# Performance work log

Hardware: AMD Instinct MI355X
Metric: run time of the kernel (lower is better)

## Reference

```python
import jax, jax.numpy as jnp
import numpy as np

B, I, H = 256, 512, 512

def setup_inputs() -> dict:
    key = jax.random.key(0)
    ks = jax.random.split(key, 12)
    u = lambda k, s: jax.random.uniform(k, s, dtype=jnp.float32)
    inp = {
        'inputs': jax.random.normal(ks[0], (B, I), dtype=jnp.float32),
        'state': jax.random.normal(ks[1], (B, H), dtype=jnp.float32),
        'sensory_mu': u(ks[2], (I, H)) * 0.5 + 0.3,
        'sensory_sigma': u(ks[3], (I, H)) * 5.0 + 3.0,
        'sensory_W': u(ks[4], (I, H)) * 0.99 + 0.01,
        'sensory_erev': (2.0 * jax.random.randint(ks[5], (I, H), 0, 2) - 1.0).astype(jnp.float32),
        'mu': u(ks[6], (H, H)) * 0.5 + 0.3,
        'sigma': u(ks[7], (H, H)) * 5.0 + 3.0,
        'W': u(ks[8], (H, H)) * 0.99 + 0.01,
        'erev': (2.0 * jax.random.randint(ks[9], (H, H), 0, 2) - 1.0).astype(jnp.float32),
        'vleak': u(ks[10], (H,)) * 0.4 - 0.2,
        'gleak': jnp.ones((H,), dtype=jnp.float32),
        'cm': jnp.full((H,), 0.5, dtype=jnp.float32),
    }
    return inp


def reference(inputs, state, sensory_mu, sensory_sigma, sensory_W, sensory_erev,
              mu, sigma, W, erev, vleak, gleak, cm):
    eps = 1e-08
    # sensory synapses: (B, I, H) broadcast
    s_act = jax.nn.sigmoid((inputs[:, :, None] - sensory_mu[None]) * sensory_sigma[None])
    s_w_act = sensory_W * s_act                      # (B, I, H)
    w_num_s = jnp.sum(s_w_act * sensory_erev, axis=1)  # (B, H)
    w_den_s = jnp.sum(s_w_act, axis=1)                 # (B, H)
    # inter-neuron synapses: (B, H, H) broadcast
    i_act = jax.nn.sigmoid((state[:, :, None] - mu[None]) * sigma[None])
    i_w_act = W * i_act                               # (B, H, H)
    w_num_i = jnp.sum(i_w_act * erev, axis=1)         # (B, H)
    w_den_i = jnp.sum(i_w_act, axis=1)                # (B, H)
    w_numerator = w_num_i + w_num_s
    w_denominator = w_den_i + w_den_s
    G_total = gleak + w_denominator
    tau = cm / (G_total + eps)
    numerator = cm * state + gleak * vleak + w_numerator
    denominator = cm + G_total
    v_inf = numerator / (denominator + eps)
    dt = 0.1
    next_state = v_inf + (state - v_inf) * jnp.exp(-dt / (tau + eps))
    return jnp.tanh(next_state)
```

## Files before the change

kernel.cpp:

```cpp
#include <hip/hip_runtime.h>
#include <stdint.h>

constexpr int NB = 256;
constexpr int NI = 512;
constexpr int NH = 512;

constexpr int TB    = 8;
constexpr int NT    = 32;
constexpr int CHUNK = 32;
constexpr int NSPL  = 32;
constexpr int HBLK  = 256;

__device__ __constant__ const float SC0 =  0.24781886f;
__device__ __constant__ const float SC1 = -0.01739900f;
__device__ __constant__ const float SC2 =  9.68558e-4f;
__device__ __constant__ const float SC3 = -3.09967e-5f;
__device__ __constant__ const float SC4 =  5.03772e-7f;
__device__ __constant__ const float SC5 = -3.21180e-9f;

__global__ __launch_bounds__(256, 6) void ltc_accum(
    const float* __restrict__ inputs,
    const float* __restrict__ state,
    const float* __restrict__ smu, const float* __restrict__ ssg,
    const float* __restrict__ sW,  const float* __restrict__ ser,
    const float* __restrict__ imu, const float* __restrict__ isg,
    const float* __restrict__ iW,  const float* __restrict__ ier,
    float* __restrict__ wsNum, float* __restrict__ wsDen)
{
    __shared__ float xs[CHUNK][TB];

    const int bi    = blockIdx.x;
    const int sigma = bi & (NSPL - 1);
    const int btile = (bi >> 5) & (NT - 1);
    const int hhalf = bi >> 10;
    const int b0 = btile * TB;
    const int h  = hhalf * HBLK + threadIdx.x;

    const bool sens = sigma < 16;
    const int  r0   = (sens ? sigma : sigma - 16) * CHUNK;

    const float* __restrict__ src  = sens ? inputs : state;
    const float* __restrict__ Pmu  = sens ? smu : imu;
    const float* __restrict__ Psg  = sens ? ssg : isg;
    const float* __restrict__ PW   = sens ? sW  : iW;
    const float* __restrict__ Per  = sens ? ser : ier;

    {
        const int ii = threadIdx.x >> 3, bb = threadIdx.x & (TB - 1);
        xs[ii][bb] = src[(b0 + bb) * 512 + r0 + ii];
    }
    __syncthreads();

    float numA[TB], denA[TB];
#pragma unroll
    for (int bb = 0; bb < TB; ++bb) { numA[bb] = 0.f; denA[bb] = 0.f; }
    float sWsum = 0.f, sWesum = 0.f;

#pragma unroll 2
    for (int ii = 0; ii < CHUNK; ++ii) {
        const int p = (r0 + ii) * NH + h;
        const float a  = Psg[p];
        const float c  = Pmu[p] * a;
        const float W  = PW[p];
        const float We = W * Per[p];
        sWsum  += W;
        sWesum += We;
#pragma unroll
        for (int bb = 0; bb < TB; ++bb) {
            const float z  = __builtin_fmaf(xs[ii][bb], a, -c);
            const float zc = fminf(fmaxf(z, -7.0f), 7.0f);
            const float s  = zc * zc;
            float pl = __builtin_fmaf(SC5, s, SC4);
            pl = __builtin_fmaf(pl, s, SC3);
            pl = __builtin_fmaf(pl, s, SC2);
            pl = __builtin_fmaf(pl, s, SC1);
            pl = __builtin_fmaf(pl, s, SC0);
            const float g = zc * pl;
            denA[bb] = __builtin_fmaf(W,  g, denA[bb]);
            numA[bb] = __builtin_fmaf(We, g, numA[bb]);
        }
    }

#pragma unroll
    for (int bb = 0; bb < TB; ++bb) {
        const float den = __builtin_fmaf(0.5f, sWsum,  denA[bb]);
        const float num = __builtin_fmaf(0.5f, sWesum, numA[bb]);
        unsafeAtomicAdd(&wsNum[(b0 + bb) * NH + h], num);
        unsafeAtomicAdd(&wsDen[(b0 + bb) * NH + h], den);
    }
}

__global__ __launch_bounds__(256) void ltc_epilogue(
    const float* __restrict__ state,
    const float* __restrict__ vleak, const float* __restrict__ gleak,
    const float* __restrict__ cm,
    const float* __restrict__ wsNum, const float* __restrict__ wsDen,
    float* __restrict__ out)
{
    const int t = blockIdx.x * 256 + threadIdx.x;
    const int h = t & (NH - 1);
    const float st = state[t];
    const float gl = gleak[h];
    const float vl = vleak[h];
    const float c  = cm[h];
    const float wnum = wsNum[t];
    const float wden = wsDen[t];
    const float eps = 1e-8f;
    const float G = gl + wden;
    const float tau = c / (G + eps);
    const float numerator = c * st + gl * vl + wnum;
    const float denominator = c + G;
    const float v_inf = numerator / (denominator + eps);
    const float next = v_inf + (st - v_inf) * expf(-0.1f / (tau + eps));
    out[t] = tanhf(next);
}

extern "C" void kernel_launch(void* const* d_in, const int* in_sizes, int n_in,
                              void* d_out, int out_size, void* d_ws, size_t ws_size,
                              hipStream_t stream) {
    const float* inputs = (const float*)d_in[0];
    const float* state  = (const float*)d_in[1];
    const float* smu    = (const float*)d_in[2];
    const float* ssg    = (const float*)d_in[3];
    const float* sW     = (const float*)d_in[4];
    const float* ser    = (const float*)d_in[5];
    const float* imu    = (const float*)d_in[6];
    const float* isg    = (const float*)d_in[7];
    const float* iW     = (const float*)d_in[8];
    const float* ier    = (const float*)d_in[9];
    const float* vleak  = (const float*)d_in[10];
    const float* gleak  = (const float*)d_in[11];
    const float* cm     = (const float*)d_in[12];

    float* wsNum = (float*)d_ws;
    float* wsDen = wsNum + NB * NH;

    hipMemsetAsync(d_ws, 0, 2ull * NB * NH * sizeof(float), stream);

    ltc_accum<<<dim3(NSPL * NT * 2), dim3(256), 0, stream>>>(
        inputs, state, smu, ssg, sW, ser, imu, isg, iW, ier, wsNum, wsDen);
    ltc_epilogue<<<dim3(NB * NH / 256), dim3(256), 0, stream>>>(
        state, vleak, gleak, cm, wsNum, wsDen, (float*)d_out);
}
```

Measured before the change: 123.2 us.

## Pack synapse parameters into float4 with precomputed mu*sigma and W*erev

Adds a pre-pass kernel that interleaves sigma, mu*sigma, W and W*erev into one float4 array per side, so the accumulate kernel issues a single 16-byte load per row instead of four scalar loads plus two multiplies. It also replaces the min/max clamp with a med3 builtin. The pack runs on every call, adding an extra read of all parameters and a 8 MB write to workspace, plus one more launch.

```diff
diff --git a/kernel.cpp b/kernel.cpp
--- a/kernel.cpp
+++ b/kernel.cpp
@@ -10,6 +10,7 @@
 constexpr int CHUNK = 32;
 constexpr int NSPL  = 32;
 constexpr int HBLK  = 256;
+constexpr int SIDE_ELEMS = 512 * 512;
 
 __device__ __constant__ const float SC0 =  0.24781886f;
 __device__ __constant__ const float SC1 = -0.01739900f;
@@ -18,13 +19,41 @@
 __device__ __constant__ const float SC4 =  5.03772e-7f;
 __device__ __constant__ const float SC5 = -3.21180e-9f;
 
-__global__ __launch_bounds__(256, 6) void ltc_accum(
-    const float* __restrict__ inputs,
-    const float* __restrict__ state,
+__device__ __forceinline__ float clamp7(float z) {
+#if __has_builtin(__builtin_amdgcn_fmed3f)
+    return __builtin_amdgcn_fmed3f(z, -7.0f, 7.0f);
+#else
+    return fminf(fmaxf(z, -7.0f), 7.0f);
+#endif
+}
+
+__global__ __launch_bounds__(256) void ltc_pack(
     const float* __restrict__ smu, const float* __restrict__ ssg,
     const float* __restrict__ sW,  const float* __restrict__ ser,
     const float* __restrict__ imu, const float* __restrict__ isg,
     const float* __restrict__ iW,  const float* __restrict__ ier,
+    float4* __restrict__ ppk)
+{
+    const int side = blockIdx.x >> 10;
+    const int e    = (blockIdx.x & 1023) * 256 + threadIdx.x;
+    const float* mu = side ? imu : smu;
+    const float* sg = side ? isg : ssg;
+    const float* W  = side ? iW  : sW;
+    const float* er = side ? ier : ser;
+    const float a  = sg[e];
+    const float w  = W[e];
+    float4 p;
+    p.x = a;
+    p.y = mu[e] * a;
+    p.z = w;
+    p.w = w * er[e];
+    ppk[side * SIDE_ELEMS + e] = p;
+}
+
+__global__ __launch_bounds__(256, 6) void ltc_accum(
+    const float* __restrict__ inputs,
+    const float* __restrict__ state,
+    const float4* __restrict__ ppk,
     float* __restrict__ wsNum, float* __restrict__ wsDen)
 {
     __shared__ float xs[CHUNK][TB];
@@ -39,11 +68,8 @@
     const bool sens = sigma < 16;
     const int  r0   = (sens ? sigma : sigma - 16) * CHUNK;
 
-    const float* __restrict__ src  = sens ? inputs : state;
-    const float* __restrict__ Pmu  = sens ? smu : imu;
-    const float* __restrict__ Psg  = sens ? ssg : isg;
-    const float* __restrict__ PW   = sens ? sW  : iW;
-    const float* __restrict__ Per  = sens ? ser : ier;
+    const float*  __restrict__ src = sens ? inputs : state;
+    const float4* __restrict__ Pp  = ppk + (sens ? 0 : SIDE_ELEMS);
 
     {
         const int ii = threadIdx.x >> 3, bb = threadIdx.x & (TB - 1);
@@ -58,17 +84,14 @@
 
 #pragma unroll 2
     for (int ii = 0; ii < CHUNK; ++ii) {
-        const int p = (r0 + ii) * NH + h;
-        const float a  = Psg[p];
-        const float c  = Pmu[p] * a;
-        const float W  = PW[p];
-        const float We = W * Per[p];
+        const float4 P = Pp[(r0 + ii) * NH + h];
+        const float a = P.x, c = P.y, W = P.z, We = P.w;
         sWsum  += W;
         sWesum += We;
 #pragma unroll
         for (int bb = 0; bb < TB; ++bb) {
             const float z  = __builtin_fmaf(xs[ii][bb], a, -c);
-            const float zc = fminf(fmaxf(z, -7.0f), 7.0f);
+            const float zc = clamp7(z);
             const float s  = zc * zc;
             float pl = __builtin_fmaf(SC5, s, SC4);
             pl = __builtin_fmaf(pl, s, SC3);
@@ -132,13 +155,16 @@
     const float* gleak  = (const float*)d_in[11];
     const float* cm     = (const float*)d_in[12];
 
-    float* wsNum = (float*)d_ws;
-    float* wsDen = wsNum + NB * NH;
+    float4* ppk   = (float4*)d_ws;
+    float*  wsNum = (float*)((char*)d_ws + 2ull * SIDE_ELEMS * sizeof(float4));
+    float*  wsDen = wsNum + NB * NH;
 
-    hipMemsetAsync(d_ws, 0, 2ull * NB * NH * sizeof(float), stream);
+    hipMemsetAsync((void*)wsNum, 0, 2ull * NB * NH * sizeof(float), stream);
 
+    ltc_pack<<<dim3(2048), dim3(256), 0, stream>>>(
+        smu, ssg, sW, ser, imu, isg, iW, ier, ppk);
     ltc_accum<<<dim3(NSPL * NT * 2), dim3(256), 0, stream>>>(
-        inputs, state, smu, ssg, sW, ser, imu, isg, iW, ier, wsNum, wsDen);
+        inputs, state, ppk, wsNum, wsDen);
     ltc_epilogue<<<dim3(NB * NH / 256), dim3(256), 0, stream>>>(
         state, vleak, gleak, cm, wsNum, wsDen, (float*)d_out);
 }
```

New measurement: 129.4 us. +5.0%, slower.

## Replace atomic accumulation with per-split partial buffers reduced in epilogue

Applied to the files above, without the earlier changes.

Drops the workspace memset and the float atomics. Each split block now writes its (num, den) partial sums as a float2 into its own workspace slice, and the epilogue sums the S slices before the final state update. The split count is picked from the workspace size, and blocks loop over several chunks when S is below 32. It also uses fmed3 for the clamp and raises the launch-bounds occupancy hint to 8. The cost is extra partial-buffer traffic, which can reach 32 MB of writes and reads when S is 32.

```diff
diff --git a/kernel.cpp b/kernel.cpp
--- a/kernel.cpp
+++ b/kernel.cpp
@@ -2,13 +2,11 @@
 #include <stdint.h>
 
 constexpr int NB = 256;
-constexpr int NI = 512;
 constexpr int NH = 512;
+constexpr int NTGT = NB * NH;
 
 constexpr int TB    = 8;
-constexpr int NT    = 32;
 constexpr int CHUNK = 32;
-constexpr int NSPL  = 32;
 constexpr int HBLK  = 256;
 
 __device__ __constant__ const float SC0 =  0.24781886f;
@@ -18,93 +16,115 @@
 __device__ __constant__ const float SC4 =  5.03772e-7f;
 __device__ __constant__ const float SC5 = -3.21180e-9f;
 
-__global__ __launch_bounds__(256, 6) void ltc_accum(
+__device__ __forceinline__ float clamp7(float z) {
+#if __has_builtin(__builtin_amdgcn_fmed3f)
+    return __builtin_amdgcn_fmed3f(z, -7.0f, 7.0f);
+#else
+    return fminf(fmaxf(z, -7.0f), 7.0f);
+#endif
+}
+
+__global__ __launch_bounds__(256, 8) void ltc_accum(
     const float* __restrict__ inputs,
     const float* __restrict__ state,
     const float* __restrict__ smu, const float* __restrict__ ssg,
     const float* __restrict__ sW,  const float* __restrict__ ser,
     const float* __restrict__ imu, const float* __restrict__ isg,
     const float* __restrict__ iW,  const float* __restrict__ ier,
-    float* __restrict__ wsNum, float* __restrict__ wsDen)
+    float2* __restrict__ part,
+    int sBits, int CPB)
 {
     __shared__ float xs[CHUNK][TB];
 
     const int bi    = blockIdx.x;
-    const int sigma = bi & (NSPL - 1);
-    const int btile = (bi >> 5) & (NT - 1);
-    const int hhalf = bi >> 10;
+    const int S     = 1 << sBits;
+    const int s     = bi & (S - 1);
+    const int rest  = bi >> sBits;
+    const int btile = rest & 31;
+    const int hhalf = rest >> 5;
     const int b0 = btile * TB;
     const int h  = hhalf * HBLK + threadIdx.x;
-
-    const bool sens = sigma < 16;
-    const int  r0   = (sens ? sigma : sigma - 16) * CHUNK;
-
-    const float* __restrict__ src  = sens ? inputs : state;
-    const float* __restrict__ Pmu  = sens ? smu : imu;
-    const float* __restrict__ Psg  = sens ? ssg : isg;
-    const float* __restrict__ PW   = sens ? sW  : iW;
-    const float* __restrict__ Per  = sens ? ser : ier;
-
-    {
-        const int ii = threadIdx.x >> 3, bb = threadIdx.x & (TB - 1);
-        xs[ii][bb] = src[(b0 + bb) * 512 + r0 + ii];
-    }
-    __syncthreads();
+    const int g0 = s * (CPB * CHUNK);
 
     float numA[TB], denA[TB];
 #pragma unroll
     for (int bb = 0; bb < TB; ++bb) { numA[bb] = 0.f; denA[bb] = 0.f; }
     float sWsum = 0.f, sWesum = 0.f;
 
+    for (int c = 0; c < CPB; ++c) {
+        const int g    = g0 + c * CHUNK;
+        const bool sens = g < 512;
+        const int  r0   = g & 511;
+
+        const float* __restrict__ src = sens ? inputs : state;
+        const float* __restrict__ Pmu = sens ? smu : imu;
+        const float* __restrict__ Psg = sens ? ssg : isg;
+        const float* __restrict__ PW  = sens ? sW  : iW;
+        const float* __restrict__ Per = sens ? ser : ier;
+
+        if (c) __syncthreads();
+        {
+            const int bb = threadIdx.x >> 5, ii = threadIdx.x & 31;
+            const float v = src[(b0 + bb) * 512 + r0 + ii];
+            xs[ii][bb] = v;
+        }
+        __syncthreads();
+
 #pragma unroll 2
-    for (int ii = 0; ii < CHUNK; ++ii) {
-        const int p = (r0 + ii) * NH + h;
-        const float a  = Psg[p];
-        const float c  = Pmu[p] * a;
-        const float W  = PW[p];
-        const float We = W * Per[p];
-        sWsum  += W;
-        sWesum += We;
+        for (int ii = 0; ii < CHUNK; ++ii) {
+            const int p = (r0 + ii) * NH + h;
+            const float a  = Psg[p];
+            const float cc = Pmu[p] * a;
+            const float W  = PW[p];
+            const float We = W * Per[p];
+            sWsum  += W;
+            sWesum += We;
 #pragma unroll
-        for (int bb = 0; bb < TB; ++bb) {
-            const float z  = __builtin_fmaf(xs[ii][bb], a, -c);
-            const float zc = fminf(fmaxf(z, -7.0f), 7.0f);
-            const float s  = zc * zc;
-            float pl = __builtin_fmaf(SC5, s, SC4);
-            pl = __builtin_fmaf(pl, s, SC3);
-            pl = __builtin_fmaf(pl, s, SC2);
-            pl = __builtin_fmaf(pl, s, SC1);
-            pl = __builtin_fmaf(pl, s, SC0);
-            const float g = zc * pl;
-            denA[bb] = __builtin_fmaf(W,  g, denA[bb]);
-            numA[bb] = __builtin_fmaf(We, g, numA[bb]);
+            for (int bb = 0; bb < TB; ++bb) {
+                const float z  = __builtin_fmaf(xs[ii][bb], a, -cc);
+                const float zc = clamp7(z);
+                const float sq = zc * zc;
+                float pl = __builtin_fmaf(SC5, sq, SC4);
+                pl = __builtin_fmaf(pl, sq, SC3);
+                pl = __builtin_fmaf(pl, sq, SC2);
+                pl = __builtin_fmaf(pl, sq, SC1);
+                pl = __builtin_fmaf(pl, sq, SC0);
+                const float gg = zc * pl;
+                denA[bb] = __builtin_fmaf(W,  gg, denA[bb]);
+                numA[bb] = __builtin_fmaf(We, gg, numA[bb]);
+            }
         }
     }
 
+    float2* __restrict__ slice = part + (size_t)s * NTGT;
 #pragma unroll
     for (int bb = 0; bb < TB; ++bb) {
         const float den = __builtin_fmaf(0.5f, sWsum,  denA[bb]);
         const float num = __builtin_fmaf(0.5f, sWesum, numA[bb]);
-        unsafeAtomicAdd(&wsNum[(b0 + bb) * NH + h], num);
-        unsafeAtomicAdd(&wsDen[(b0 + bb) * NH + h], den);
+        slice[(b0 + bb) * NH + h] = make_float2(num, den);
     }
 }
 
-__global__ __launch_bounds__(256) void ltc_epilogue(
+__global__ __launch_bounds__(256) void ltc_reduce_epilogue(
     const float* __restrict__ state,
     const float* __restrict__ vleak, const float* __restrict__ gleak,
     const float* __restrict__ cm,
-    const float* __restrict__ wsNum, const float* __restrict__ wsDen,
+    const float2* __restrict__ part, int S,
     float* __restrict__ out)
 {
     const int t = blockIdx.x * 256 + threadIdx.x;
     const int h = t & (NH - 1);
+
+    float wnum = 0.f, wden = 0.f;
+    for (int s = 0; s < S; ++s) {
+        const float2 p = part[(size_t)s * NTGT + t];
+        wnum += p.x; wden += p.y;
+    }
+
     const float st = state[t];
     const float gl = gleak[h];
     const float vl = vleak[h];
     const float c  = cm[h];
-    const float wnum = wsNum[t];
-    const float wden = wsDen[t];
     const float eps = 1e-8f;
     const float G = gl + wden;
     const float tau = c / (G + eps);
@@ -132,13 +152,17 @@
     const float* gleak  = (const float*)d_in[11];
     const float* cm     = (const float*)d_in[12];
 
-    float* wsNum = (float*)d_ws;
-    float* wsDen = wsNum + NB * NH;
+    int sBits;
+    if      (ws_size >= 32ull * NTGT * sizeof(float2)) sBits = 5;
+    else if (ws_size >= 16ull * NTGT * sizeof(float2)) sBits = 4;
+    else                                               sBits = 3;
+    const int S   = 1 << sBits;
+    const int CPB = 32 / S;
 
-    hipMemsetAsync(d_ws, 0, 2ull * NB * NH * sizeof(float), stream);
+    float2* part = (float2*)d_ws;
 
-    ltc_accum<<<dim3(NSPL * NT * 2), dim3(256), 0, stream>>>(
-        inputs, state, smu, ssg, sW, ser, imu, isg, iW, ier, wsNum, wsDen);
-    ltc_epilogue<<<dim3(NB * NH / 256), dim3(256), 0, stream>>>(
-        state, vleak, gleak, cm, wsNum, wsDen, (float*)d_out);
+    ltc_accum<<<dim3(S * 64), dim3(256), 0, stream>>>(
+        inputs, state, smu, ssg, sW, ser, imu, isg, iW, ier, part, sBits, CPB);
+    ltc_reduce_epilogue<<<dim3(NTGT / 256), dim3(256), 0, stream>>>(
+        state, vleak, gleak, cm, part, S, (float*)d_out);
 }
```

New measurement: 127.2 us. 1.03x slower.
